# Optimization experiments

Hardware: AMD Instinct MI355X
Metric: run time of the kernel (lower is better)

The kernel has to match this reference:

```python
import jax, jax.numpy as jnp
import numpy as np
import math

D_INNER = 1024
D_STATE = 16
DT_RANK = 64  # d_inner // 16


def setup_inputs() -> dict:
    key = jax.random.key(0)
    ks = jax.random.split(key, 8)
    B, L, M, D, R = 2, 2048, D_INNER, D_STATE, DT_RANK
    x = jax.random.normal(ks[0], (B, L, M), dtype=jnp.float32)
    z = jax.random.normal(ks[1], (B, L, M), dtype=jnp.float32)
    # Parameters (torch Linear weight layout: [out, in])
    x_proj_w = jax.random.normal(ks[2], (R + 2 * D, M), dtype=jnp.float32) / jnp.sqrt(M)
    dt_init_std = R ** (-0.5)
    dt_proj_w = jax.random.uniform(ks[3], (M, R), dtype=jnp.float32, minval=-dt_init_std, maxval=dt_init_std)
    dt_min, dt_max = 0.001, 0.1
    dt = jnp.exp(jax.random.uniform(ks[4], (M,), dtype=jnp.float32) * (math.log(dt_max) - math.log(dt_min)) + math.log(dt_min))
    dt_proj_b = dt + jnp.log(-jnp.expm1(-dt))  # inverse softplus init
    A_log = jax.random.normal(ks[5], (D, M), dtype=jnp.float32) * 0.1
    D_param = jnp.ones((M,), dtype=jnp.float32)
    return {"x": x, "z": z, "x_proj_w": x_proj_w, "dt_proj_w": dt_proj_w,
            "dt_proj_b": dt_proj_b, "A_log": A_log, "D_param": D_param}


def reference(x, z, x_proj_w, dt_proj_w, dt_proj_b, A_log, D_param):
    B, L, M = x.shape
    D = A_log.shape[0]
    R = dt_proj_w.shape[1]
    # Input-dependent projections
    xp = jnp.einsum('blm,nm->bln', x, x_proj_w)          # [B,L,R+2D]
    dt_in = xp[..., :R]
    B_ssm = xp[..., R:R + D]                              # [B,L,D]
    C_ssm = xp[..., R + D:]                               # [B,L,D]
    dt = jax.nn.softplus(jnp.einsum('blr,mr->blm', dt_in, dt_proj_w) + dt_proj_b)  # [B,L,M]
    A = -jnp.exp(A_log).T                                 # [M,D]

    def step(h, inp):
        dt_t, x_t, B_t, C_t = inp                         # [B,M],[B,M],[B,D],[B,D]
        dA = jnp.exp(dt_t[:, :, None] * A[None])          # [B,M,D]
        h = dA * h + (dt_t * x_t)[:, :, None] * B_t[:, None, :]
        y_t = jnp.einsum('bmd,bd->bm', h, C_t) + D_param * x_t
        return h, y_t

    h0 = jnp.zeros((B, M, D), dtype=x.dtype)
    xs = (jnp.swapaxes(dt, 0, 1), jnp.swapaxes(x, 0, 1),
          jnp.swapaxes(B_ssm, 0, 1), jnp.swapaxes(C_ssm, 0, 1))
    _, ys = jax.lax.scan(step, h0, xs)                    # ys: [L,B,M]
    y = jnp.swapaxes(ys, 0, 1)
    y = y * jax.nn.silu(z)
    return y
```

## Files before the change

kernel.cpp:

```cpp
#include <hip/hip_runtime.h>
#include <math.h>

#define BB 2
#define LL 2048
#define MM 1024
#define DD 16
#define RR 64
#define NN 96
#define BLROWS (BB*LL)
#define NCH 64
#define CLEN (LL/NCH)

#define LOG2E 1.44269504088896340736f

#define OFF_XP    0
#define OFF_DT    (OFF_XP + BLROWS*NN)
#define OFF_A2    (OFF_DT + BLROWS*MM/2)
#define OFF_HEND  (OFF_A2 + MM*DD)
#define OFF_DTSUM (OFF_HEND + NCH*BB*MM*DD)

typedef __attribute__((ext_vector_type(8))) short bf16x8;
typedef __attribute__((ext_vector_type(4))) float f32x4;
typedef __attribute__((ext_vector_type(4))) unsigned short u16x4;

union BF8 { bf16x8 v; unsigned u[4]; };

__device__ __forceinline__ unsigned cvtpk(float a, float b) {
  unsigned r;
  asm("v_cvt_pk_bf16_f32 %0, %1, %2" : "=v"(r) : "v"(a), "v"(b));
  return r;
}

__device__ __forceinline__ float vexp2(float x) {
  float r;
  asm("v_exp_f32 %0, %1" : "=v"(r) : "v"(x));
  return r;
}

__device__ __forceinline__ float softplusf(float v) {
  return v > 20.f ? v : __logf(1.f + __expf(v));
}

__device__ __forceinline__ short f2bf(float f) {
  union { float f; unsigned u; } v; v.f = f;
  unsigned r = v.u + 0x7FFFu + ((v.u >> 16) & 1u);
  return (short)(r >> 16);
}

__device__ __forceinline__ float bf2f(unsigned short u) {
  return __uint_as_float((unsigned)u << 16);
}

__device__ __forceinline__ float dpp_xor1(float v) {
  int i = __builtin_amdgcn_mov_dpp(__float_as_int(v), 0xB1, 0xF, 0xF, true);
  return __int_as_float(i);
}
__device__ __forceinline__ float dpp_xor2(float v) {
  int i = __builtin_amdgcn_mov_dpp(__float_as_int(v), 0x4E, 0xF, 0xF, true);
  return __int_as_float(i);
}

#define XP_GEMM_BLOCKS ((BLROWS/16)*3)
__global__ __launch_bounds__(64) void k_xp(const float* __restrict__ x,
                                           const float* __restrict__ W,
                                           const float* __restrict__ A_log,
                                           float* __restrict__ ws) {
  if (blockIdx.x >= XP_GEMM_BLOCKS) {
    int idx = (blockIdx.x - XP_GEMM_BLOCKS) * 64 + threadIdx.x;
    int m = idx >> 4, d = idx & 15;
    ws[OFF_A2 + idx] = -__expf(A_log[d * MM + m]) * LOG2E;
    return;
  }
  float* xp = ws + OFF_XP;
  int lane = threadIdx.x;
  int rt = blockIdx.x / 3, np = blockIdx.x % 3;
  int lr = lane & 15, lk = lane >> 4;
  const float* xr = x + (size_t)(rt * 16 + lr) * MM + lk * 8;
  const float* wr0 = W + (size_t)(np * 32 + lr) * MM + lk * 8;
  const float* wr1 = W + (size_t)(np * 32 + 16 + lr) * MM + lk * 8;
  f32x4 acc0 = {0.f, 0.f, 0.f, 0.f}, acc1 = {0.f, 0.f, 0.f, 0.f};
#pragma unroll 2
  for (int kk = 0; kk < MM; kk += 32) {
    float4 xa = *(const float4*)(xr + kk);
    float4 xb = *(const float4*)(xr + kk + 4);
    float4 p0 = *(const float4*)(wr0 + kk);
    float4 p1 = *(const float4*)(wr0 + kk + 4);
    float4 q0 = *(const float4*)(wr1 + kk);
    float4 q1 = *(const float4*)(wr1 + kk + 4);
    BF8 a, b0, b1;
    a.u[0] = cvtpk(xa.x, xa.y); a.u[1] = cvtpk(xa.z, xa.w);
    a.u[2] = cvtpk(xb.x, xb.y); a.u[3] = cvtpk(xb.z, xb.w);
    b0.u[0] = cvtpk(p0.x, p0.y); b0.u[1] = cvtpk(p0.z, p0.w);
    b0.u[2] = cvtpk(p1.x, p1.y); b0.u[3] = cvtpk(p1.z, p1.w);
    b1.u[0] = cvtpk(q0.x, q0.y); b1.u[1] = cvtpk(q0.z, q0.w);
    b1.u[2] = cvtpk(q1.x, q1.y); b1.u[3] = cvtpk(q1.z, q1.w);
    acc0 = __builtin_amdgcn_mfma_f32_16x16x32_bf16(a.v, b0.v, acc0, 0, 0, 0);
    acc1 = __builtin_amdgcn_mfma_f32_16x16x32_bf16(a.v, b1.v, acc1, 0, 0, 0);
  }
  int r0 = rt * 16 + lk * 4, c0 = np * 32 + lr;
#pragma unroll
  for (int e = 0; e < 4; ++e) {
    xp[(size_t)(r0 + e) * NN + c0] = acc0[e];
    xp[(size_t)(r0 + e) * NN + c0 + 16] = acc1[e];
  }
}

__global__ __launch_bounds__(64) void k_dt(const float* __restrict__ dtW,
                                           const float* __restrict__ dtb,
                                           float* __restrict__ ws) {
  const float* xp = ws + OFF_XP;
  unsigned short* dt16 = (unsigned short*)(ws + OFF_DT);
  int lane = threadIdx.x;
  int rt = blockIdx.x >> 3, mg = blockIdx.x & 7;
  int lr = lane & 15, lk = lane >> 4;
  const float* xr = xp + (size_t)(rt * 16 + lr) * NN + lk * 8;
  BF8 a0, a1;
  {
    float4 xa = *(const float4*)(xr);
    float4 xb = *(const float4*)(xr + 4);
    float4 xc = *(const float4*)(xr + 32);
    float4 xd = *(const float4*)(xr + 36);
    a0.u[0] = cvtpk(xa.x, xa.y); a0.u[1] = cvtpk(xa.z, xa.w);
    a0.u[2] = cvtpk(xb.x, xb.y); a0.u[3] = cvtpk(xb.z, xb.w);
    a1.u[0] = cvtpk(xc.x, xc.y); a1.u[1] = cvtpk(xc.z, xc.w);
    a1.u[2] = cvtpk(xd.x, xd.y); a1.u[3] = cvtpk(xd.z, xd.w);
  }
  int r0 = rt * 16 + lk * 4;
#pragma unroll 2
  for (int mt = 0; mt < 8; ++mt) {
    int mcol = (mg * 8 + mt) * 16 + lr;
    const float* wr = dtW + (size_t)mcol * RR + lk * 8;
    float4 p0 = *(const float4*)(wr);
    float4 p1 = *(const float4*)(wr + 4);
    float4 p2 = *(const float4*)(wr + 32);
    float4 p3 = *(const float4*)(wr + 36);
    BF8 b0, b1;
    b0.u[0] = cvtpk(p0.x, p0.y); b0.u[1] = cvtpk(p0.z, p0.w);
    b0.u[2] = cvtpk(p1.x, p1.y); b0.u[3] = cvtpk(p1.z, p1.w);
    b1.u[0] = cvtpk(p2.x, p2.y); b1.u[1] = cvtpk(p2.z, p2.w);
    b1.u[2] = cvtpk(p3.x, p3.y); b1.u[3] = cvtpk(p3.z, p3.w);
    f32x4 acc = {0.f, 0.f, 0.f, 0.f};
    acc = __builtin_amdgcn_mfma_f32_16x16x32_bf16(a0.v, b0.v, acc, 0, 0, 0);
    acc = __builtin_amdgcn_mfma_f32_16x16x32_bf16(a1.v, b1.v, acc, 0, 0, 0);
    float bv = dtb[mcol];
#pragma unroll
    for (int e = 0; e < 4; ++e)
      dt16[(size_t)(r0 + e) * MM + mcol] = (unsigned short)f2bf(softplusf(acc[e] + bv));
  }
}

__global__ __launch_bounds__(256) void k_scan1(const float* __restrict__ x,
                                               float* __restrict__ ws) {
  const float* xp = ws + OFF_XP;
  const float* A2t = ws + OFF_A2;
  float* hend = ws + OFF_HEND;
  float* dtsum = ws + OFF_DTSUM;
  __shared__ __align__(16) float ds_[CLEN * 64];
  __shared__ __align__(16) float xs_[CLEN * 64];
  __shared__ __align__(16) float bs[CLEN * DD];
  int wg = blockIdx.x;
  int mw = wg & 15, c = (wg >> 4) & (NCH - 1), b = wg >> 10;
  int t = threadIdx.x;
  int ml = t >> 2, dsub = t & 3;
  int m0 = mw * 64, m = m0 + ml;
  int l0 = c * CLEN;
  const unsigned short* dtg = (const unsigned short*)(ws + OFF_DT) + (size_t)(b * LL + l0) * MM + m0;
  const float* xg = x + (size_t)(b * LL + l0) * MM + m0;
#pragma unroll
  for (int i = t; i < CLEN * 16; i += 256) {
    int lo = i >> 4, q = i & 15;
    u16x4 dv = *(const u16x4*)&dtg[(size_t)lo * MM + q * 4];
    *(float4*)&ds_[lo * 64 + q * 4] = make_float4(bf2f(dv[0]), bf2f(dv[1]), bf2f(dv[2]), bf2f(dv[3]));
    *(float4*)&xs_[lo * 64 + q * 4] = *(const float4*)&xg[(size_t)lo * MM + q * 4];
  }
  for (int i = t; i < CLEN * DD; i += 256) {
    int r = i >> 4, cc = i & 15;
    bs[i] = xp[(size_t)(b * LL + l0 + r) * NN + RR + cc];
  }
  __syncthreads();
  float4 A2v = *(const float4*)&A2t[m * DD + dsub * 4];
  float h0_ = 0.f, h1_ = 0.f, h2_ = 0.f, h3_ = 0.f, S = 0.f;
#pragma unroll 4
  for (int lo = 0; lo < CLEN; ++lo) {
    float dtv = ds_[lo * 64 + ml];
    float xv = xs_[lo * 64 + ml];
    float4 Bv = *(const float4*)&bs[lo * DD + dsub * 4];
    S += dtv;
    float dtx = dtv * xv;
    h0_ = vexp2(dtv * A2v.x) * h0_ + dtx * Bv.x;
    h1_ = vexp2(dtv * A2v.y) * h1_ + dtx * Bv.y;
    h2_ = vexp2(dtv * A2v.z) * h2_ + dtx * Bv.z;
    h3_ = vexp2(dtv * A2v.w) * h3_ + dtx * Bv.w;
  }
  size_t o = ((size_t)((c * BB + b) * MM + m)) * DD + dsub * 4;
  *(float4*)&hend[o] = make_float4(h0_, h1_, h2_, h3_);
  if (dsub == 0) dtsum[(c * BB + b) * MM + m] = S;
}

__global__ __launch_bounds__(256) void k_scan2(float* __restrict__ ws) {
  int t = blockIdx.x * 256 + threadIdx.x;
  int d = t & 15, m = (t >> 4) & 1023, b = t >> 14;
  float* hend = ws + OFF_HEND;
  const float* dtsum = ws + OFF_DTSUM;
  float A2 = ws[OFF_A2 + m * DD + d];
  const size_t hstride = (size_t)BB * MM * DD;
  const int sstride = BB * MM;
  size_t o = ((size_t)b * MM + m) * DD + d;
  int si = b * MM + m;
  float h = 0.f;
  float he = hend[o], S = dtsum[si];
  for (int c = 0; c < NCH; ++c) {
    float heN = 0.f, SN = 0.f;
    if (c + 1 < NCH) {
      heN = hend[o + hstride];
      SN = dtsum[si + sstride];
    }
    hend[o] = h;
    h = vexp2(A2 * S) * h + he;
    he = heN; S = SN;
    o += hstride; si += sstride;
  }
}

__global__ __launch_bounds__(256) void k_scan3(const float* __restrict__ x,
                                               const float* __restrict__ z,
                                               const float* __restrict__ Dp,
                                               float* __restrict__ out,
                                               float* __restrict__ ws) {
  const float* xp = ws + OFF_XP;
  const float* A2t = ws + OFF_A2;
  const float* h0w = ws + OFF_HEND;
  __shared__ __align__(16) float ds_[CLEN * 64];
  __shared__ __align__(16) float xs_[CLEN * 64];
  __shared__ __align__(16) float zs_[CLEN * 64];
  __shared__ __align__(16) float bs[CLEN * 32];
  int wg = blockIdx.x;
  int mw = wg & 15, c = (wg >> 4) & (NCH - 1), b = wg >> 10;
  int t = threadIdx.x;
  int ml = t >> 2, dsub = t & 3;
  int m0 = mw * 64, m = m0 + ml;
  int l0 = c * CLEN;
  const unsigned short* dtg = (const unsigned short*)(ws + OFF_DT) + (size_t)(b * LL + l0) * MM + m0;
  const float* xg = x + (size_t)(b * LL + l0) * MM + m0;
  const float* zg = z + (size_t)(b * LL + l0) * MM + m0;
#pragma unroll
  for (int i = t; i < CLEN * 16; i += 256) {
    int lo = i >> 4, q = i & 15;
    u16x4 dv = *(const u16x4*)&dtg[(size_t)lo * MM + q * 4];
    *(float4*)&ds_[lo * 64 + q * 4] = make_float4(bf2f(dv[0]), bf2f(dv[1]), bf2f(dv[2]), bf2f(dv[3]));
    *(float4*)&xs_[lo * 64 + q * 4] = *(const float4*)&xg[(size_t)lo * MM + q * 4];
    *(float4*)&zs_[lo * 64 + q * 4] = *(const float4*)&zg[(size_t)lo * MM + q * 4];
  }
  for (int i = t; i < CLEN * 32; i += 256) {
    int r = i >> 5, cc = i & 31;
    bs[i] = xp[(size_t)(b * LL + l0 + r) * NN + RR + cc];
  }
  __syncthreads();
  float4 A2v = *(const float4*)&A2t[m * DD + dsub * 4];
  size_t o = ((size_t)((c * BB + b) * MM + m)) * DD + dsub * 4;
  float4 hv = *(const float4*)&h0w[o];
  float h0_ = hv.x, h1_ = hv.y, h2_ = hv.z, h3_ = hv.w;
  float Dpm = Dp[m];
  size_t idx = ((size_t)(b * LL + l0)) * MM + m;
#pragma unroll 4
  for (int lo = 0; lo < CLEN; ++lo) {
    float dtv = ds_[lo * 64 + ml];
    float xv = xs_[lo * 64 + ml];
    float zv = zs_[lo * 64 + ml];
    float4 Bv = *(const float4*)&bs[lo * 32 + dsub * 4];
    float4 Cv = *(const float4*)&bs[lo * 32 + DD + dsub * 4];
    float dtx = dtv * xv;
    h0_ = vexp2(dtv * A2v.x) * h0_ + dtx * Bv.x;
    h1_ = vexp2(dtv * A2v.y) * h1_ + dtx * Bv.y;
    h2_ = vexp2(dtv * A2v.z) * h2_ + dtx * Bv.z;
    h3_ = vexp2(dtv * A2v.w) * h3_ + dtx * Bv.w;
    float yp = h0_ * Cv.x + h1_ * Cv.y + h2_ * Cv.z + h3_ * Cv.w;
    yp += dpp_xor1(yp);
    yp += dpp_xor2(yp);
    float sig = __builtin_amdgcn_rcpf(1.f + vexp2(-LOG2E * zv));
    if (dsub == 0)
      out[idx + (size_t)lo * MM] = (yp + Dpm * xv) * zv * sig;
  }
}

extern "C" void kernel_launch(void* const* d_in, const int* in_sizes, int n_in,
                              void* d_out, int out_size, void* d_ws, size_t ws_size,
                              hipStream_t stream) {
  const float* x = (const float*)d_in[0];
  const float* z = (const float*)d_in[1];
  const float* W = (const float*)d_in[2];
  const float* dtW = (const float*)d_in[3];
  const float* dtb = (const float*)d_in[4];
  const float* A_log = (const float*)d_in[5];
  const float* Dp = (const float*)d_in[6];
  float* out = (float*)d_out;
  float* ws = (float*)d_ws;

  k_xp<<<XP_GEMM_BLOCKS + (MM * DD / 64), 64, 0, stream>>>(x, W, A_log, ws);
  k_dt<<<(BLROWS / 16) * 8, 64, 0, stream>>>(dtW, dtb, ws);
  k_scan1<<<16 * NCH * BB, 256, 0, stream>>>(x, ws);
  k_scan2<<<128, 256, 0, stream>>>(ws);
  k_scan3<<<16 * NCH * BB, 256, 0, stream>>>(x, z, Dp, out, ws);
}
```

Before: 81.89 us.

## Give each scan thread eight states and pack dt and x as bf16 in LDS

The two chunked scan kernels now map two threads per channel, each holding eight state elements, so a block covers 128 channels and the grid is halved. The per-channel work (dt/x loads, sigmoid, D*x term) is amortised over more states, and the output reduction needs one DPP step instead of two. dt and x are stored together as one packed bf16 pair per LDS word, which shrinks shared memory traffic and footprint. The cost is that x is rounded to bf16, which reduces accuracy in both the state update and the skip term. It also leaves fewer threads per block to hide latency.

```diff
diff --git a/kernel.cpp b/kernel.cpp
--- a/kernel.cpp
+++ b/kernel.cpp
@@ -23,7 +23,7 @@
 typedef __attribute__((ext_vector_type(4))) float f32x4;
 typedef __attribute__((ext_vector_type(4))) unsigned short u16x4;
 
-union BF8 { bf16x8 v; unsigned u[4]; };
+union BF8 { bf16x8 v; unsigned u[4]; uint4 q; };
 
 __device__ __forceinline__ unsigned cvtpk(float a, float b) {
   unsigned r;
@@ -47,16 +47,8 @@
   return (short)(r >> 16);
 }
 
-__device__ __forceinline__ float bf2f(unsigned short u) {
-  return __uint_as_float((unsigned)u << 16);
-}
-
 __device__ __forceinline__ float dpp_xor1(float v) {
   int i = __builtin_amdgcn_mov_dpp(__float_as_int(v), 0xB1, 0xF, 0xF, true);
-  return __int_as_float(i);
-}
-__device__ __forceinline__ float dpp_xor2(float v) {
-  int i = __builtin_amdgcn_mov_dpp(__float_as_int(v), 0x4E, 0xF, 0xF, true);
   return __int_as_float(i);
 }
 
@@ -155,45 +147,60 @@
   const float* A2t = ws + OFF_A2;
   float* hend = ws + OFF_HEND;
   float* dtsum = ws + OFF_DTSUM;
-  __shared__ __align__(16) float ds_[CLEN * 64];
-  __shared__ __align__(16) float xs_[CLEN * 64];
+  __shared__ __align__(16) unsigned dtxs[CLEN * 128];
   __shared__ __align__(16) float bs[CLEN * DD];
   int wg = blockIdx.x;
-  int mw = wg & 15, c = (wg >> 4) & (NCH - 1), b = wg >> 10;
+  int mw = wg & 7, c = (wg >> 3) & (NCH - 1), b = wg >> 9;
   int t = threadIdx.x;
-  int ml = t >> 2, dsub = t & 3;
-  int m0 = mw * 64, m = m0 + ml;
+  int ml = t >> 1, dsub = t & 1;
+  int m0 = mw * 128, m = m0 + ml;
   int l0 = c * CLEN;
   const unsigned short* dtg = (const unsigned short*)(ws + OFF_DT) + (size_t)(b * LL + l0) * MM + m0;
   const float* xg = x + (size_t)(b * LL + l0) * MM + m0;
 #pragma unroll
-  for (int i = t; i < CLEN * 16; i += 256) {
-    int lo = i >> 4, q = i & 15;
+  for (int i = t; i < CLEN * 32; i += 256) {
+    int lo = i >> 5, q = i & 31;
     u16x4 dv = *(const u16x4*)&dtg[(size_t)lo * MM + q * 4];
-    *(float4*)&ds_[lo * 64 + q * 4] = make_float4(bf2f(dv[0]), bf2f(dv[1]), bf2f(dv[2]), bf2f(dv[3]));
-    *(float4*)&xs_[lo * 64 + q * 4] = *(const float4*)&xg[(size_t)lo * MM + q * 4];
-  }
+    float4 xv = *(const float4*)&xg[(size_t)lo * MM + q * 4];
+    unsigned xp01 = cvtpk(xv.x, xv.y), xp23 = cvtpk(xv.z, xv.w);
+    uint4 o;
+    o.x = ((xp01 & 0xffffu) << 16) | (unsigned)dv[0];
+    o.y = (xp01 & 0xffff0000u) | (unsigned)dv[1];
+    o.z = ((xp23 & 0xffffu) << 16) | (unsigned)dv[2];
+    o.w = (xp23 & 0xffff0000u) | (unsigned)dv[3];
+    *(uint4*)&dtxs[lo * 128 + q * 4] = o;
+  }
+#pragma unroll
   for (int i = t; i < CLEN * DD; i += 256) {
     int r = i >> 4, cc = i & 15;
     bs[i] = xp[(size_t)(b * LL + l0 + r) * NN + RR + cc];
   }
   __syncthreads();
-  float4 A2v = *(const float4*)&A2t[m * DD + dsub * 4];
-  float h0_ = 0.f, h1_ = 0.f, h2_ = 0.f, h3_ = 0.f, S = 0.f;
+  float4 A2a = *(const float4*)&A2t[m * DD + dsub * 8];
+  float4 A2b = *(const float4*)&A2t[m * DD + dsub * 8 + 4];
+  float h0_ = 0.f, h1_ = 0.f, h2_ = 0.f, h3_ = 0.f;
+  float h4_ = 0.f, h5_ = 0.f, h6_ = 0.f, h7_ = 0.f, S = 0.f;
 #pragma unroll 4
   for (int lo = 0; lo < CLEN; ++lo) {
-    float dtv = ds_[lo * 64 + ml];
-    float xv = xs_[lo * 64 + ml];
-    float4 Bv = *(const float4*)&bs[lo * DD + dsub * 4];
+    unsigned p = dtxs[lo * 128 + ml];
+    float dtv = __uint_as_float(p << 16);
+    float xv = __uint_as_float(p & 0xffff0000u);
+    float4 B0 = *(const float4*)&bs[lo * DD + dsub * 8];
+    float4 B1 = *(const float4*)&bs[lo * DD + dsub * 8 + 4];
     S += dtv;
     float dtx = dtv * xv;
-    h0_ = vexp2(dtv * A2v.x) * h0_ + dtx * Bv.x;
-    h1_ = vexp2(dtv * A2v.y) * h1_ + dtx * Bv.y;
-    h2_ = vexp2(dtv * A2v.z) * h2_ + dtx * Bv.z;
-    h3_ = vexp2(dtv * A2v.w) * h3_ + dtx * Bv.w;
-  }
-  size_t o = ((size_t)((c * BB + b) * MM + m)) * DD + dsub * 4;
+    h0_ = vexp2(dtv * A2a.x) * h0_ + dtx * B0.x;
+    h1_ = vexp2(dtv * A2a.y) * h1_ + dtx * B0.y;
+    h2_ = vexp2(dtv * A2a.z) * h2_ + dtx * B0.z;
+    h3_ = vexp2(dtv * A2a.w) * h3_ + dtx * B0.w;
+    h4_ = vexp2(dtv * A2b.x) * h4_ + dtx * B1.x;
+    h5_ = vexp2(dtv * A2b.y) * h5_ + dtx * B1.y;
+    h6_ = vexp2(dtv * A2b.z) * h6_ + dtx * B1.z;
+    h7_ = vexp2(dtv * A2b.w) * h7_ + dtx * B1.w;
+  }
+  size_t o = ((size_t)((c * BB + b) * MM + m)) * DD + dsub * 8;
   *(float4*)&hend[o] = make_float4(h0_, h1_, h2_, h3_);
+  *(float4*)&hend[o + 4] = make_float4(h4_, h5_, h6_, h7_);
   if (dsub == 0) dtsum[(c * BB + b) * MM + m] = S;
 }
 
@@ -230,53 +237,69 @@
   const float* xp = ws + OFF_XP;
   const float* A2t = ws + OFF_A2;
   const float* h0w = ws + OFF_HEND;
-  __shared__ __align__(16) float ds_[CLEN * 64];
-  __shared__ __align__(16) float xs_[CLEN * 64];
-  __shared__ __align__(16) float zs_[CLEN * 64];
+  __shared__ __align__(16) unsigned dtxs[CLEN * 128];
+  __shared__ __align__(16) float zs_[CLEN * 128];
   __shared__ __align__(16) float bs[CLEN * 32];
   int wg = blockIdx.x;
-  int mw = wg & 15, c = (wg >> 4) & (NCH - 1), b = wg >> 10;
+  int mw = wg & 7, c = (wg >> 3) & (NCH - 1), b = wg >> 9;
   int t = threadIdx.x;
-  int ml = t >> 2, dsub = t & 3;
-  int m0 = mw * 64, m = m0 + ml;
+  int ml = t >> 1, dsub = t & 1;
+  int m0 = mw * 128, m = m0 + ml;
   int l0 = c * CLEN;
   const unsigned short* dtg = (const unsigned short*)(ws + OFF_DT) + (size_t)(b * LL + l0) * MM + m0;
   const float* xg = x + (size_t)(b * LL + l0) * MM + m0;
   const float* zg = z + (size_t)(b * LL + l0) * MM + m0;
 #pragma unroll
-  for (int i = t; i < CLEN * 16; i += 256) {
-    int lo = i >> 4, q = i & 15;
+  for (int i = t; i < CLEN * 32; i += 256) {
+    int lo = i >> 5, q = i & 31;
     u16x4 dv = *(const u16x4*)&dtg[(size_t)lo * MM + q * 4];
-    *(float4*)&ds_[lo * 64 + q * 4] = make_float4(bf2f(dv[0]), bf2f(dv[1]), bf2f(dv[2]), bf2f(dv[3]));
-    *(float4*)&xs_[lo * 64 + q * 4] = *(const float4*)&xg[(size_t)lo * MM + q * 4];
-    *(float4*)&zs_[lo * 64 + q * 4] = *(const float4*)&zg[(size_t)lo * MM + q * 4];
-  }
+    float4 xv = *(const float4*)&xg[(size_t)lo * MM + q * 4];
+    unsigned xp01 = cvtpk(xv.x, xv.y), xp23 = cvtpk(xv.z, xv.w);
+    uint4 o;
+    o.x = ((xp01 & 0xffffu) << 16) | (unsigned)dv[0];
+    o.y = (xp01 & 0xffff0000u) | (unsigned)dv[1];
+    o.z = ((xp23 & 0xffffu) << 16) | (unsigned)dv[2];
+    o.w = (xp23 & 0xffff0000u) | (unsigned)dv[3];
+    *(uint4*)&dtxs[lo * 128 + q * 4] = o;
+    *(float4*)&zs_[lo * 128 + q * 4] = *(const float4*)&zg[(size_t)lo * MM + q * 4];
+  }
+#pragma unroll
   for (int i = t; i < CLEN * 32; i += 256) {
     int r = i >> 5, cc = i & 31;
     bs[i] = xp[(size_t)(b * LL + l0 + r) * NN + RR + cc];
   }
   __syncthreads();
-  float4 A2v = *(const float4*)&A2t[m * DD + dsub * 4];
-  size_t o = ((size_t)((c * BB + b) * MM + m)) * DD + dsub * 4;
-  float4 hv = *(const float4*)&h0w[o];
-  float h0_ = hv.x, h1_ = hv.y, h2_ = hv.z, h3_ = hv.w;
+  float4 A2a = *(const float4*)&A2t[m * DD + dsub * 8];
+  float4 A2b = *(const float4*)&A2t[m * DD + dsub * 8 + 4];
+  size_t o = ((size_t)((c * BB + b) * MM + m)) * DD + dsub * 8;
+  float4 hva = *(const float4*)&h0w[o];
+  float4 hvb = *(const float4*)&h0w[o + 4];
+  float h0_ = hva.x, h1_ = hva.y, h2_ = hva.z, h3_ = hva.w;
+  float h4_ = hvb.x, h5_ = hvb.y, h6_ = hvb.z, h7_ = hvb.w;
   float Dpm = Dp[m];
   size_t idx = ((size_t)(b * LL + l0)) * MM + m;
 #pragma unroll 4
   for (int lo = 0; lo < CLEN; ++lo) {
-    float dtv = ds_[lo * 64 + ml];
-    float xv = xs_[lo * 64 + ml];
-    float zv = zs_[lo * 64 + ml];
-    float4 Bv = *(const float4*)&bs[lo * 32 + dsub * 4];
-    float4 Cv = *(const float4*)&bs[lo * 32 + DD + dsub * 4];
+    unsigned p = dtxs[lo * 128 + ml];
+    float dtv = __uint_as_float(p << 16);
+    float xv = __uint_as_float(p & 0xffff0000u);
+    float zv = zs_[lo * 128 + ml];
+    float4 B0 = *(const float4*)&bs[lo * 32 + dsub * 8];
+    float4 B1 = *(const float4*)&bs[lo * 32 + dsub * 8 + 4];
+    float4 C0 = *(const float4*)&bs[lo * 32 + DD + dsub * 8];
+    float4 C1 = *(const float4*)&bs[lo * 32 + DD + dsub * 8 + 4];
     float dtx = dtv * xv;
-    h0_ = vexp2(dtv * A2v.x) * h0_ + dtx * Bv.x;
-    h1_ = vexp2(dtv * A2v.y) * h1_ + dtx * Bv.y;
-    h2_ = vexp2(dtv * A2v.z) * h2_ + dtx * Bv.z;
-    h3_ = vexp2(dtv * A2v.w) * h3_ + dtx * Bv.w;
-    float yp = h0_ * Cv.x + h1_ * Cv.y + h2_ * Cv.z + h3_ * Cv.w;
+    h0_ = vexp2(dtv * A2a.x) * h0_ + dtx * B0.x;
+    h1_ = vexp2(dtv * A2a.y) * h1_ + dtx * B0.y;
+    h2_ = vexp2(dtv * A2a.z) * h2_ + dtx * B0.z;
+    h3_ = vexp2(dtv * A2a.w) * h3_ + dtx * B0.w;
+    h4_ = vexp2(dtv * A2b.x) * h4_ + dtx * B1.x;
+    h5_ = vexp2(dtv * A2b.y) * h5_ + dtx * B1.y;
+    h6_ = vexp2(dtv * A2b.z) * h6_ + dtx * B1.z;
+    h7_ = vexp2(dtv * A2b.w) * h7_ + dtx * B1.w;
+    float yp = h0_ * C0.x + h1_ * C0.y + h2_ * C0.z + h3_ * C0.w
+             + h4_ * C1.x + h5_ * C1.y + h6_ * C1.z + h7_ * C1.w;
     yp += dpp_xor1(yp);
-    yp += dpp_xor2(yp);
     float sig = __builtin_amdgcn_rcpf(1.f + vexp2(-LOG2E * zv));
     if (dsub == 0)
       out[idx + (size_t)lo * MM] = (yp + Dpm * xv) * zv * sig;
@@ -298,7 +321,7 @@
 
   k_xp<<<XP_GEMM_BLOCKS + (MM * DD / 64), 64, 0, stream>>>(x, W, A_log, ws);
   k_dt<<<(BLROWS / 16) * 8, 64, 0, stream>>>(dtW, dtb, ws);
-  k_scan1<<<16 * NCH * BB, 256, 0, stream>>>(x, ws);
+  k_scan1<<<8 * NCH * BB, 256, 0, stream>>>(x, ws);
   k_scan2<<<128, 256, 0, stream>>>(ws);
-  k_scan3<<<16 * NCH * BB, 256, 0, stream>>>(x, z, Dp, out, ws);
-}
+  k_scan3<<<8 * NCH * BB, 256, 0, stream>>>(x, z, Dp, out, ws);
+}
```

New measurement: 83.51 us. Within noise of the previous version (+2.0%).
